# Kernel optimization log

Measured on AMD Instinct MI355X. Metric: run time of the kernel, lower is better.

Reference implementation:

```python
import jax, jax.numpy as jnp
import numpy as np

FORCE = 8.0
N_STATE = 40
BATCH = 524288


def setup_inputs() -> dict:
    key = jax.random.key(0)
    x0 = jax.random.normal(key, (BATCH, N_STATE), dtype=jnp.float32)
    t = jnp.float32(0.0)          # unused: system is autonomous (torch code passes nan)
    dt = jnp.float32(0.05)        # canonical Lorenz96 RK4 step
    return {"x0": x0, "t": t, "dt": dt}


def _dxdt(x):
    # torch shift(x, n) == roll(x, -n, dims=-1)
    # dxdt = (shift(x,1) - shift(x,-2)) * shift(x,-1) - x + force
    return (jnp.roll(x, -1, axis=-1) - jnp.roll(x, 2, axis=-1)) * jnp.roll(x, 1, axis=-1) - x + FORCE


def reference(x0, t, dt):
    # Classic RK4 step (rk4_torch); t is ignored (autonomous RHS).
    k1 = _dxdt(x0)
    k2 = _dxdt(x0 + 0.5 * dt * k1)
    k3 = _dxdt(x0 + 0.5 * dt * k2)
    k4 = _dxdt(x0 + dt * k3)
    return x0 + (dt / 6.0) * (k1 + 2.0 * k2 + 2.0 * k3 + k4)
```

## Files before the change

### kernel.cpp

```cpp
#include <hip/hip_runtime.h>


#define N_STATE 40
#define FORCE 8.0f

__global__ __launch_bounds__(256)
void lorenz96_rk4_kernel(const float* __restrict__ x0,
                         const float* __restrict__ dt_p,
                         float* __restrict__ out,
                         int batch)
{
    int row = blockIdx.x * blockDim.x + threadIdx.x;
    if (row >= batch) return;

    const float dt = dt_p[0];
    const float hdt = 0.5f * dt;

    const float* xp = x0 + (size_t)row * N_STATE;
    float*       op = out + (size_t)row * N_STATE;

    float x[N_STATE];
    #pragma unroll
    for (int j = 0; j < N_STATE / 4; ++j) {
        float4 v = ((const float4*)xp)[j];
        x[4 * j + 0] = v.x;
        x[4 * j + 1] = v.y;
        x[4 * j + 2] = v.z;
        x[4 * j + 3] = v.w;
    }

    float acc[N_STATE];
    float a[N_STATE];
    float b[N_STATE];

    #pragma unroll
    for (int i = 0; i < N_STATE; ++i) {
        float k = (x[(i + 1) % N_STATE] - x[(i + 38) % N_STATE])
                  * x[(i + 39) % N_STATE] - x[i] + FORCE;
        acc[i] = k;
        a[i] = x[i] + hdt * k;
    }
    #pragma unroll
    for (int i = 0; i < N_STATE; ++i) {
        float k = (a[(i + 1) % N_STATE] - a[(i + 38) % N_STATE])
                  * a[(i + 39) % N_STATE] - a[i] + FORCE;
        acc[i] += 2.0f * k;
        b[i] = x[i] + hdt * k;
    }
    #pragma unroll
    for (int i = 0; i < N_STATE; ++i) {
        float k = (b[(i + 1) % N_STATE] - b[(i + 38) % N_STATE])
                  * b[(i + 39) % N_STATE] - b[i] + FORCE;
        acc[i] += 2.0f * k;
        a[i] = x[i] + dt * k;
    }
    #pragma unroll
    for (int i = 0; i < N_STATE; ++i) {
        float k = (a[(i + 1) % N_STATE] - a[(i + 38) % N_STATE])
                  * a[(i + 39) % N_STATE] - a[i] + FORCE;
        acc[i] += k;
    }

    const float s = dt * (1.0f / 6.0f);
    #pragma unroll
    for (int j = 0; j < N_STATE / 4; ++j) {
        float4 v;
        v.x = x[4 * j + 0] + s * acc[4 * j + 0];
        v.y = x[4 * j + 1] + s * acc[4 * j + 1];
        v.z = x[4 * j + 2] + s * acc[4 * j + 2];
        v.w = x[4 * j + 3] + s * acc[4 * j + 3];
        ((float4*)op)[j] = v;
    }
}

extern "C" void kernel_launch(void* const* d_in, const int* in_sizes, int n_in,
                              void* d_out, int out_size, void* d_ws, size_t ws_size,
                              hipStream_t stream) {
    const float* x0 = (const float*)d_in[0];
    const float* dt = (const float*)d_in[2];
    float* out = (float*)d_out;

    int batch = in_sizes[0] / N_STATE;
    int block = 256;
    int grid = (batch + block - 1) / block;
    lorenz96_rk4_kernel<<<grid, block, 0, stream>>>(x0, dt, out, batch);
}
```

Before: 180.6 us.

## Split each row across ten lanes with wavefront shuffles for halo exchange

Instead of one thread holding a full 40-element row in registers, each wavefront processes 6 rows with 10 lanes per row, each lane owning one float4. Neighbor values needed by the Lorenz96 stencil are exchanged with __shfl at each RK4 stage. This cuts register pressure and raises occupancy, and it makes the global loads coalesced across adjacent lanes instead of each thread striding over its own 160 bytes. The cost is 4 idle lanes per wave and 12 shuffles per thread.

```diff
diff --git a/kernel.cpp b/kernel.cpp
--- a/kernel.cpp
+++ b/kernel.cpp
@@ -1,87 +1,84 @@
 #include <hip/hip_runtime.h>
 
 
-#define N_STATE 40
 #define FORCE 8.0f
 
 __global__ __launch_bounds__(256)
-void lorenz96_rk4_kernel(const float* __restrict__ x0,
-                         const float* __restrict__ dt_p,
-                         float* __restrict__ out,
-                         int batch)
+void lorenz96_rk4_shfl(const float4* __restrict__ x0,
+                       const float* __restrict__ dt_p,
+                       float4* __restrict__ out,
+                       long nf4)
 {
-    int row = blockIdx.x * blockDim.x + threadIdx.x;
-    if (row >= batch) return;
+    const long tid  = (long)blockIdx.x * blockDim.x + threadIdx.x;
+    const long wave = tid >> 6;
+    const int  lane = (int)(tid & 63);
+    const int  lrow = lane / 10;
+    const int  c    = lane - lrow * 10;
+    const long f    = wave * 60 + lane;
+    const bool active = (lane < 60) && (f < nf4);
 
-    const float dt = dt_p[0];
+    const int lL = lrow * 10 + (c == 0 ? 9 : c - 1);
+    const int lR = lrow * 10 + (c == 9 ? 0 : c + 1);
+
+    const float dt  = dt_p[0];
     const float hdt = 0.5f * dt;
 
-    const float* xp = x0 + (size_t)row * N_STATE;
-    float*       op = out + (size_t)row * N_STATE;
+    float4 v = make_float4(0.f, 0.f, 0.f, 0.f);
+    if (active) v = x0[f];
+    const float x0r = v.x, x1r = v.y, x2r = v.z, x3r = v.w;
 
-    float x[N_STATE];
-    #pragma unroll
-    for (int j = 0; j < N_STATE / 4; ++j) {
-        float4 v = ((const float4*)xp)[j];
-        x[4 * j + 0] = v.x;
-        x[4 * j + 1] = v.y;
-        x[4 * j + 2] = v.z;
-        x[4 * j + 3] = v.w;
-    }
+    auto deriv = [&](float s0, float s1, float s2, float s3,
+                     float& d0, float& d1, float& d2, float& d3) {
+        float hL2 = __shfl(s2, lL);
+        float hL3 = __shfl(s3, lL);
+        float hR0 = __shfl(s0, lR);
+        d0 = (s1  - hL2) * hL3 - s0 + FORCE;
+        d1 = (s2  - hL3) * s0  - s1 + FORCE;
+        d2 = (s3  - s0 ) * s1  - s2 + FORCE;
+        d3 = (hR0 - s1 ) * s2  - s3 + FORCE;
+    };
 
-    float acc[N_STATE];
-    float a[N_STATE];
-    float b[N_STATE];
+    float k0, k1, k2, k3;
+    float a0, a1, a2, a3;
+    float y0, y1, y2, y3;
 
-    #pragma unroll
-    for (int i = 0; i < N_STATE; ++i) {
-        float k = (x[(i + 1) % N_STATE] - x[(i + 38) % N_STATE])
-                  * x[(i + 39) % N_STATE] - x[i] + FORCE;
-        acc[i] = k;
-        a[i] = x[i] + hdt * k;
-    }
-    #pragma unroll
-    for (int i = 0; i < N_STATE; ++i) {
-        float k = (a[(i + 1) % N_STATE] - a[(i + 38) % N_STATE])
-                  * a[(i + 39) % N_STATE] - a[i] + FORCE;
-        acc[i] += 2.0f * k;
-        b[i] = x[i] + hdt * k;
-    }
-    #pragma unroll
-    for (int i = 0; i < N_STATE; ++i) {
-        float k = (b[(i + 1) % N_STATE] - b[(i + 38) % N_STATE])
-                  * b[(i + 39) % N_STATE] - b[i] + FORCE;
-        acc[i] += 2.0f * k;
-        a[i] = x[i] + dt * k;
-    }
-    #pragma unroll
-    for (int i = 0; i < N_STATE; ++i) {
-        float k = (a[(i + 1) % N_STATE] - a[(i + 38) % N_STATE])
-                  * a[(i + 39) % N_STATE] - a[i] + FORCE;
-        acc[i] += k;
-    }
+    deriv(x0r, x1r, x2r, x3r, k0, k1, k2, k3);
+    a0 = k0; a1 = k1; a2 = k2; a3 = k3;
+    y0 = x0r + hdt * k0; y1 = x1r + hdt * k1;
+    y2 = x2r + hdt * k2; y3 = x3r + hdt * k3;
+
+    deriv(y0, y1, y2, y3, k0, k1, k2, k3);
+    a0 += 2.0f * k0; a1 += 2.0f * k1; a2 += 2.0f * k2; a3 += 2.0f * k3;
+    y0 = x0r + hdt * k0; y1 = x1r + hdt * k1;
+    y2 = x2r + hdt * k2; y3 = x3r + hdt * k3;
+
+    deriv(y0, y1, y2, y3, k0, k1, k2, k3);
+    a0 += 2.0f * k0; a1 += 2.0f * k1; a2 += 2.0f * k2; a3 += 2.0f * k3;
+    y0 = x0r + dt * k0; y1 = x1r + dt * k1;
+    y2 = x2r + dt * k2; y3 = x3r + dt * k3;
+
+    deriv(y0, y1, y2, y3, k0, k1, k2, k3);
+    a0 += k0; a1 += k1; a2 += k2; a3 += k3;
 
     const float s = dt * (1.0f / 6.0f);
-    #pragma unroll
-    for (int j = 0; j < N_STATE / 4; ++j) {
-        float4 v;
-        v.x = x[4 * j + 0] + s * acc[4 * j + 0];
-        v.y = x[4 * j + 1] + s * acc[4 * j + 1];
-        v.z = x[4 * j + 2] + s * acc[4 * j + 2];
-        v.w = x[4 * j + 3] + s * acc[4 * j + 3];
-        ((float4*)op)[j] = v;
-    }
+    float4 r;
+    r.x = x0r + s * a0;
+    r.y = x1r + s * a1;
+    r.z = x2r + s * a2;
+    r.w = x3r + s * a3;
+    if (active) out[f] = r;
 }
 
 extern "C" void kernel_launch(void* const* d_in, const int* in_sizes, int n_in,
                               void* d_out, int out_size, void* d_ws, size_t ws_size,
                               hipStream_t stream) {
-    const float* x0 = (const float*)d_in[0];
+    const float4* x0 = (const float4*)d_in[0];
     const float* dt = (const float*)d_in[2];
-    float* out = (float*)d_out;
+    float4* out = (float4*)d_out;
 
-    int batch = in_sizes[0] / N_STATE;
-    int block = 256;
-    int grid = (batch + block - 1) / block;
-    lorenz96_rk4_kernel<<<grid, block, 0, stream>>>(x0, dt, out, batch);
+    const long nf4 = (long)in_sizes[0] / 4;
+    const long nwaves = (nf4 + 59) / 60;
+    const int block = 256;
+    const long grid = (nwaves + 3) / 4;
+    lorenz96_rk4_shfl<<<dim3((unsigned)grid), dim3(block), 0, stream>>>(x0, dt, out, nf4);
 }
```

After: 147.3 us. 18.4% less time.
